# Kernel optimization log

Measured on AMD Instinct MI355X. Metric: run time of the kernel, lower is better.

Reference implementation:

```python
import jax, jax.numpy as jnp
import numpy as np

TAU = 20.0
DECAY = 1.0 - 1.0 / TAU  # constant-coefficient leaky decay


def setup_inputs() -> dict:
    key = jax.random.key(0)
    T, B, F = 1024, 64, 1024
    inputs = jax.random.normal(key, (T, B, F), dtype=jnp.float32)
    return {"inputs": inputs}


def reference(inputs):
    # Original torch loop: new_mem = (1-1/tau)*mem + flt, where flt is the
    # PREVIOUS timestep's input (flt starts at zero, updated after mem).
    # => mem[t] = DECAY * mem[t-1] + inputs[t-1], inputs[-1] := 0, mem[-1] := 0.
    # Shift inputs by one step along time.
    x = jnp.concatenate([jnp.zeros_like(inputs[:1]), inputs[:-1]], axis=0)  # (T,B,F)
    decay = jnp.asarray(DECAY, dtype=inputs.dtype)

    def step(mem, xt):
        new_mem = decay * mem + xt
        return new_mem, new_mem

    init = jnp.zeros(inputs.shape[1:], dtype=inputs.dtype)  # (B,F)
    _, mem_rec = jax.lax.scan(step, init, x)  # (T,B,F)
    # torch: stack(dim=1) -> (B,T,F), permute(1,0,2) -> (T,B,F); scan already gives (T,B,F)
    return mem_rec
```

## Files before the change

### kernel.cpp

```cpp
#include <hip/hip_runtime.h>


#define T_DIM   1024
#define N_CH    65536
#define N4      (N_CH / 4)
#define NCHUNK  8
#define CHUNK_L 128
#define WARMUP  128

__global__ __launch_bounds__(256) void leaky_scan_kernel(
    const float4* __restrict__ in, float4* __restrict__ out)
{
    const int c = blockIdx.x * 256 + threadIdx.x;
    const int j = blockIdx.y;
    const float D = 0.95f;
    float4 m = make_float4(0.f, 0.f, 0.f, 0.f);

    if (j == 0) {
        out[c] = m;
        const float4* p = in + c;
        float4* q = out + (size_t)N4 + c;
        #pragma unroll 8
        for (int t = 1; t < CHUNK_L; ++t) {
            float4 v = *p;
            m.x = fmaf(D, m.x, v.x);
            m.y = fmaf(D, m.y, v.y);
            m.z = fmaf(D, m.z, v.z);
            m.w = fmaf(D, m.w, v.w);
            *q = m;
            p += N4; q += N4;
        }
    } else {
        const int t0 = j * CHUNK_L;
        const int w = (t0 - 1 < WARMUP) ? (t0 - 1) : WARMUP;
        const float4* p = in + (size_t)(t0 - w - 1) * N4 + c;
        #pragma unroll 8
        for (int t = 0; t < w; ++t) {
            float4 v = *p;
            m.x = fmaf(D, m.x, v.x);
            m.y = fmaf(D, m.y, v.y);
            m.z = fmaf(D, m.z, v.z);
            m.w = fmaf(D, m.w, v.w);
            p += N4;
        }
        float4* q = out + (size_t)t0 * N4 + c;
        #pragma unroll 8
        for (int t = 0; t < CHUNK_L; ++t) {
            float4 v = *p;
            m.x = fmaf(D, m.x, v.x);
            m.y = fmaf(D, m.y, v.y);
            m.z = fmaf(D, m.z, v.z);
            m.w = fmaf(D, m.w, v.w);
            *q = m;
            p += N4; q += N4;
        }
    }
}

extern "C" void kernel_launch(void* const* d_in, const int* in_sizes, int n_in,
                              void* d_out, int out_size, void* d_ws, size_t ws_size,
                              hipStream_t stream)
{
    const float4* in = (const float4*)d_in[0];
    float4* out = (float4*)d_out;
    dim3 grid(N4 / 256, NCHUNK);
    leaky_scan_kernel<<<grid, dim3(256), 0, stream>>>(in, out);
}
```

Measured before the change: 541.3 us.

## Split time into more chunks, batch loads by eight, use nontemporal stores

Doubles the number of time chunks (64-step chunks instead of 128) to raise block count and occupancy, keeping the 128-step warmup. Restructures loops to issue eight independent loads before the dependent FMA chain, and writes outputs with nontemporal stores to avoid polluting cache. The warmup re-read overhead grows relative to useful work, increasing total read traffic.

```diff
diff --git a/kernel.cpp b/kernel.cpp
--- a/kernel.cpp
+++ b/kernel.cpp
@@ -4,9 +4,16 @@
 #define T_DIM   1024
 #define N_CH    65536
 #define N4      (N_CH / 4)
-#define NCHUNK  8
-#define CHUNK_L 128
+#define NCHUNK  16
+#define CHUNK_L 64
 #define WARMUP  128
+
+typedef float f32x4 __attribute__((ext_vector_type(4)));
+
+__device__ __forceinline__ void ntstore(float4* p, const float4& v) {
+    f32x4 x; x.x = v.x; x.y = v.y; x.z = v.z; x.w = v.w;
+    __builtin_nontemporal_store(x, reinterpret_cast<f32x4*>(p));
+}
 
 __global__ __launch_bounds__(256) void leaky_scan_kernel(
     const float4* __restrict__ in, float4* __restrict__ out)
@@ -15,44 +22,68 @@
     const int j = blockIdx.y;
     const float D = 0.95f;
     float4 m = make_float4(0.f, 0.f, 0.f, 0.f);
+    const int t0 = j * CHUNK_L;
+
+    const float4* p;
+    float4* q;
+    int w, nmain;
 
     if (j == 0) {
-        out[c] = m;
-        const float4* p = in + c;
-        float4* q = out + (size_t)N4 + c;
-        #pragma unroll 8
-        for (int t = 1; t < CHUNK_L; ++t) {
+        ntstore(out + c, m);
+        p = in + c;
+        q = out + (size_t)N4 + c;
+        w = 0;
+        nmain = CHUNK_L - 1;
+    } else {
+        w = t0 - 1; if (w > WARMUP) w = WARMUP;
+        p = in + (size_t)(t0 - w - 1) * N4 + c;
+        q = out + (size_t)t0 * N4 + c;
+        nmain = CHUNK_L;
+    }
+
+    {
+        const int wrem = w & 7;
+        for (int i = 0; i < wrem; ++i) {
             float4 v = *p;
-            m.x = fmaf(D, m.x, v.x);
-            m.y = fmaf(D, m.y, v.y);
-            m.z = fmaf(D, m.z, v.z);
-            m.w = fmaf(D, m.w, v.w);
-            *q = m;
+            m.x = fmaf(D, m.x, v.x); m.y = fmaf(D, m.y, v.y);
+            m.z = fmaf(D, m.z, v.z); m.w = fmaf(D, m.w, v.w);
+            p += N4;
+        }
+        const int wb = w >> 3;
+        for (int g = 0; g < wb; ++g) {
+            float4 v[8];
+            #pragma unroll
+            for (int i = 0; i < 8; ++i) v[i] = p[(size_t)i * N4];
+            #pragma unroll
+            for (int i = 0; i < 8; ++i) {
+                m.x = fmaf(D, m.x, v[i].x); m.y = fmaf(D, m.y, v[i].y);
+                m.z = fmaf(D, m.z, v[i].z); m.w = fmaf(D, m.w, v[i].w);
+            }
+            p += (size_t)8 * N4;
+        }
+    }
+
+    {
+        const int mrem = nmain & 7;
+        for (int i = 0; i < mrem; ++i) {
+            float4 v = *p;
+            m.x = fmaf(D, m.x, v.x); m.y = fmaf(D, m.y, v.y);
+            m.z = fmaf(D, m.z, v.z); m.w = fmaf(D, m.w, v.w);
+            ntstore(q, m);
             p += N4; q += N4;
         }
-    } else {
-        const int t0 = j * CHUNK_L;
-        const int w = (t0 - 1 < WARMUP) ? (t0 - 1) : WARMUP;
-        const float4* p = in + (size_t)(t0 - w - 1) * N4 + c;
-        #pragma unroll 8
-        for (int t = 0; t < w; ++t) {
-            float4 v = *p;
-            m.x = fmaf(D, m.x, v.x);
-            m.y = fmaf(D, m.y, v.y);
-            m.z = fmaf(D, m.z, v.z);
-            m.w = fmaf(D, m.w, v.w);
-            p += N4;
-        }
-        float4* q = out + (size_t)t0 * N4 + c;
-        #pragma unroll 8
-        for (int t = 0; t < CHUNK_L; ++t) {
-            float4 v = *p;
-            m.x = fmaf(D, m.x, v.x);
-            m.y = fmaf(D, m.y, v.y);
-            m.z = fmaf(D, m.z, v.z);
-            m.w = fmaf(D, m.w, v.w);
-            *q = m;
-            p += N4; q += N4;
+        const int mb = nmain >> 3;
+        for (int g = 0; g < mb; ++g) {
+            float4 v[8];
+            #pragma unroll
+            for (int i = 0; i < 8; ++i) v[i] = p[(size_t)i * N4];
+            #pragma unroll
+            for (int i = 0; i < 8; ++i) {
+                m.x = fmaf(D, m.x, v[i].x); m.y = fmaf(D, m.y, v[i].y);
+                m.z = fmaf(D, m.z, v[i].z); m.w = fmaf(D, m.w, v[i].w);
+                ntstore(q + (size_t)i * N4, m);
+            }
+            p += (size_t)8 * N4; q += (size_t)8 * N4;
         }
     }
 }
```

After: 470.2 us. -13.1%, faster.
